# Kernel optimization log

Measured on AMD Instinct MI355X. Metric: run time of the kernel, lower is better.

The kernel has to match this reference:

```python
import jax, jax.numpy as jnp
import numpy as np

T, B = 384, 128
IN_DIM, HID, OUT_DIM = 512, 1024, 512


def _lstm_step(h, c, x_t, Wx, Wh, b):
    # x_t: [B, D], h/c: [B, H]; gates order: i, f, g, o
    gates = x_t @ Wx + h @ Wh + b  # [B, 4H]
    i, f, g, o = jnp.split(gates, 4, axis=-1)
    c_new = jax.nn.sigmoid(f) * c + jax.nn.sigmoid(i) * jnp.tanh(g)
    h_new = jax.nn.sigmoid(o) * jnp.tanh(c_new)
    return h_new, c_new


def setup_inputs() -> dict:
    key = jax.random.key(0)
    ks = jax.random.split(key, 9)
    s_in = 1.0 / np.sqrt(IN_DIM)
    s_h = 1.0 / np.sqrt(HID)
    s_o = 1.0 / np.sqrt(OUT_DIM)
    return {
        "x": jax.random.normal(ks[0], (T, B, IN_DIM), dtype=jnp.float32),
        "hidden_state": jnp.zeros((1, B, HID), dtype=jnp.float32),
        "cell_state": jnp.zeros((1, B, HID), dtype=jnp.float32),
        "enc_Wx": jax.random.normal(ks[1], (IN_DIM, 4 * HID), dtype=jnp.float32) * s_in,
        "enc_Wh": jax.random.normal(ks[2], (HID, 4 * HID), dtype=jnp.float32) * s_h,
        "enc_b": jnp.zeros((4 * HID,), dtype=jnp.float32),
        "dec_Wx": jax.random.normal(ks[3], (OUT_DIM, 4 * HID), dtype=jnp.float32) * s_o,
        "dec_Wh": jax.random.normal(ks[4], (HID, 4 * HID), dtype=jnp.float32) * s_h,
        "dec_b": jnp.zeros((4 * HID,), dtype=jnp.float32),
        "fc_W": jax.random.normal(ks[5], (HID, OUT_DIM), dtype=jnp.float32) * s_h,
        "fc_b": jnp.zeros((OUT_DIM,), dtype=jnp.float32),
    }


def reference(x, hidden_state, cell_state, enc_Wx, enc_Wh, enc_b,
              dec_Wx, dec_Wh, dec_b, fc_W, fc_b):
    # ---- encoder: run LSTM over T steps, keep only final hidden state ----
    h0, c0 = hidden_state[0], cell_state[0]  # [B, H]

    def enc_step(carry, x_t):
        h, c = carry
        h, c = _lstm_step(h, c, x_t, enc_Wx, enc_Wh, enc_b)
        return (h, c), None

    (h_enc, _), _ = jax.lax.scan(enc_step, (h0, c0), x)

    y0 = jnp.zeros((B, OUT_DIM), dtype=x.dtype)
    c_dec0 = jnp.zeros((B, HID), dtype=x.dtype)

    def dec_step(carry, _):
        y, h, c = carry
        h, c = _lstm_step(h, c, y, dec_Wx, dec_Wh, dec_b)
        y = jax.nn.softmax(h @ fc_W + fc_b, axis=-1)  # softmax over dim=2
        return (y, h, c), y

    _, output = jax.lax.scan(dec_step, (y0, h_enc, c_dec0), None, length=T)
    return output  # [T, B, OUT_DIM]
```

## Files before the change

### kernel.cpp

```cpp
#include <hip/hip_runtime.h>


#define TS 384

typedef __attribute__((ext_vector_type(8))) short bf16x8;
typedef __attribute__((ext_vector_type(4))) float f32x4;

#define WS_XR 4096u
#define XR_SLOT 262144u
#define WS_HP (WS_XR + 4u*XR_SLOT)
#define HP_BUF 524288u
#define WS_FPN (WS_HP + 2u*HP_BUF)
#define WS_TOTAL (WS_FPN + 2097152u)

__device__ __forceinline__ unsigned short bf16r(float v) {
  unsigned u = __float_as_uint(v);
  u += 0x7FFFu + ((u >> 16) & 1u);
  return (unsigned short)(u >> 16);
}
__device__ __forceinline__ float bf2f(unsigned short h) {
  return __uint_as_float(((unsigned)h) << 16);
}
__device__ __forceinline__ void split2(float v, short& hi, short& lo) {
  unsigned short h = bf16r(v);
  float r = v - bf2f(h);
  hi = (short)h; lo = (short)bf16r(r);
}
__device__ __forceinline__ float sigm(float v)  { return 1.0f / (1.0f + __expf(-v)); }
__device__ __forceinline__ float tanhfa(float v){ return 1.0f - 2.0f / (__expf(2.0f*v) + 1.0f); }

__device__ __forceinline__ void st_u64(void* p, unsigned long long v) {
  __hip_atomic_store((unsigned long long*)p, v, __ATOMIC_RELAXED, __HIP_MEMORY_SCOPE_AGENT);
}
__device__ __forceinline__ void st_f32(float* p, float v) {
  __hip_atomic_store(p, v, __ATOMIC_RELAXED, __HIP_MEMORY_SCOPE_AGENT);
}
__device__ __forceinline__ float ld_f32(const float* p) {
  return __hip_atomic_load(p, __ATOMIC_RELAXED, __HIP_MEMORY_SCOPE_AGENT);
}
union FRAG { unsigned long long q[2]; bf16x8 v; };
__device__ __forceinline__ bf16x8 ld_frag(const short* base) {
  FRAG u;
  u.q[0] = __hip_atomic_load((const unsigned long long*)base, __ATOMIC_RELAXED, __HIP_MEMORY_SCOPE_AGENT);
  u.q[1] = __hip_atomic_load((const unsigned long long*)(base + 4), __ATOMIC_RELAXED, __HIP_MEMORY_SCOPE_AGENT);
  return u.v;
}

__device__ __forceinline__ void setflag(unsigned* flag, unsigned val) {
  asm volatile("s_waitcnt vmcnt(0)" ::: "memory");
  __syncthreads();
  if (threadIdx.x == 0) {
    __hip_atomic_store(flag, val, __ATOMIC_RELAXED, __HIP_MEMORY_SCOPE_AGENT);
    asm volatile("s_waitcnt vmcnt(0)" ::: "memory");
  }
}
__device__ __forceinline__ void waitflags(const unsigned* flags, int nflags,
                                          unsigned target, bool fence, int* sDead) {
  if (threadIdx.x < 64) {
    const int i = threadIdx.x;
    const bool act = (i * 4) < nflags;
    const unsigned long long* q = (const unsigned long long*)(flags + i * 4);
    unsigned spins = 0;
    for (;;) {
      bool ok = true;
      if (act) {
        unsigned long long q0 = __hip_atomic_load(q, __ATOMIC_RELAXED, __HIP_MEMORY_SCOPE_AGENT);
        unsigned long long q1 = __hip_atomic_load(q + 1, __ATOMIC_RELAXED, __HIP_MEMORY_SCOPE_AGENT);
        ok = ((unsigned)q0 >= target) && ((unsigned)(q0 >> 32) >= target)
          && ((unsigned)q1 >= target) && ((unsigned)(q1 >> 32) >= target);
      }
      if (__all(ok)) break;
      __builtin_amdgcn_s_sleep(1);
      if (++spins > (1u << 19)) { if (i == 0) *sDead = 1; break; }
    }
    if (fence) __builtin_amdgcn_fence(__ATOMIC_ACQUIRE, "agent");
  }
  __syncthreads();
}

__device__ void load_gate_weights(const float* __restrict__ Wx, const float* __restrict__ Wh,
                                  int p, short* sBh, short* sBl) {
  for (int idx = threadIdx.x; idx < 24576; idx += 1024) {
    int j = idx & 7, l = (idx >> 3) & 63, kb = idx >> 9;
    int k = kb * 32 + ((l >> 4) << 3) + j;
    int c = l & 15;
    int gcol = (c >> 2) * 1024 + p * 4 + (c & 3);
    float wv = (k < 512) ? Wx[(size_t)k * 4096 + gcol]
                         : Wh[(size_t)(k - 512) * 4096 + gcol];
    short hi, lo; split2(wv, hi, lo);
    sBh[idx] = hi; sBl[idx] = lo;
  }
}
__device__ void load_fc_weights(const float* __restrict__ fcW, int kg, int cg,
                                short* sFh, short* sFl) {
  for (int idx = threadIdx.x; idx < 4096; idx += 1024) {
    int j = idx & 7, l = (idx >> 3) & 63, kb = idx >> 9;
    int unit = kg * 256 + kb * 32 + ((l >> 4) << 3) + j;
    int col = cg * 16 + (l & 15);
    short hi, lo; split2(fcW[(size_t)unit * 512 + col], hi, lo);
    sFh[idx] = hi; sFl[idx] = lo;
  }
}

__device__ __forceinline__ void gg(const short* AHs, const short* ALs,
    const short* BHs, const short* BLs, int mt, int l,
    int kbA0, int kbB0, int nkb, f32x4* acc)
{
  const bf16x8* AH = (const bf16x8*)AHs;
  const bf16x8* AL = (const bf16x8*)ALs;
  const bf16x8* BH = (const bf16x8*)BHs;
  const bf16x8* BL = (const bf16x8*)BLs;
  #pragma unroll 2
  for (int i = 0; i < nkb; i += 2) {
    int ka = kbA0 + i, kb = kbB0 + i;
    bf16x8 ah0 = AH[(ka * 8 + mt) * 64 + l];
    bf16x8 al0 = AL[(ka * 8 + mt) * 64 + l];
    bf16x8 bh0 = BH[kb * 64 + l];
    bf16x8 bl0 = BL[kb * 64 + l];
    bf16x8 ah1 = AH[((ka + 1) * 8 + mt) * 64 + l];
    bf16x8 al1 = AL[((ka + 1) * 8 + mt) * 64 + l];
    bf16x8 bh1 = BH[(kb + 1) * 64 + l];
    bf16x8 bl1 = BL[(kb + 1) * 64 + l];
    acc[0] = __builtin_amdgcn_mfma_f32_16x16x32_bf16(ah0, bh0, acc[0], 0, 0, 0);
    acc[1] = __builtin_amdgcn_mfma_f32_16x16x32_bf16(ah0, bl0, acc[1], 0, 0, 0);
    acc[2] = __builtin_amdgcn_mfma_f32_16x16x32_bf16(al0, bh0, acc[2], 0, 0, 0);
    acc[3] = __builtin_amdgcn_mfma_f32_16x16x32_bf16(ah1, bh1, acc[3], 0, 0, 0);
    acc[4] = __builtin_amdgcn_mfma_f32_16x16x32_bf16(ah1, bl1, acc[4], 0, 0, 0);
    acc[5] = __builtin_amdgcn_mfma_f32_16x16x32_bf16(al1, bh1, acc[5], 0, 0, 0);
  }
}
__device__ __forceinline__ void gg_finish(f32x4* acc, int kh, int mt, int l,
                                          float* LDSgate) {
  f32x4 s = (acc[0] + acc[3]) + ((acc[1] + acc[4]) + (acc[2] + acc[5]));
  const int col = l & 15, r0 = mt * 16 + ((l >> 4) << 2);
  float* plane = LDSgate + kh * 2176;
  #pragma unroll
  for (int j = 0; j < 4; ++j) plane[(r0 + j) * 17 + col] = s[j];
}

__device__ __forceinline__ void conv_x(const float* __restrict__ xsrc,
                                       short* dstH, short* dstL, int p, int t) {
  if (t < 32) {
    int g = p * 32 + t;
    int l = g & 63, mt = (g >> 6) & 7, kb = g >> 9;
    int row = mt * 16 + (l & 15), k = kb * 32 + ((l >> 4) << 3);
    const float* xs = xsrc + (size_t)row * 512 + k;
    unsigned long long h64[2] = {0, 0}, l64[2] = {0, 0};
    #pragma unroll
    for (int j = 0; j < 8; ++j) {
      short hi, lo; split2(xs[j], hi, lo);
      h64[j >> 2] |= (unsigned long long)(unsigned short)hi << ((j & 3) * 16);
      l64[j >> 2] |= (unsigned long long)(unsigned short)lo << ((j & 3) * 16);
    }
    int off = g * 8;
    st_u64(dstH + off, h64[0]); st_u64(dstH + off + 4, h64[1]);
    st_u64(dstL + off, l64[0]); st_u64(dstL + off + 4, l64[1]);
  }
}

__global__ void __launch_bounds__(1024, 1)
lstm6(const float* __restrict__ x, const float* __restrict__ h0p,
      const float* __restrict__ c0p, const float* __restrict__ eWx,
      const float* __restrict__ eWh, const float* __restrict__ eb,
      const float* __restrict__ dWx, const float* __restrict__ dWh,
      const float* __restrict__ db, const float* __restrict__ fcW,
      const float* __restrict__ fcb, float* __restrict__ out,
      char* __restrict__ ws)
{
  __shared__ __align__(16) short sBh[24576], sBl[24576];
  __shared__ __align__(16) short sFh[4096], sFl[4096];
  __shared__ float LDSgate[2 * 2176];
  __shared__ unsigned hsplit[512];
  __shared__ float ybuf[512];
  __shared__ float red[16];
  __shared__ int sDead;

  const int p = blockIdx.x, t = threadIdx.x;
  const int w = t >> 6, l = t & 63;
  const int mt = w & 7, kh = w >> 3;
  if (t == 0) sDead = 0;

  unsigned* hflag = (unsigned*)ws;
  unsigned* yflag = (unsigned*)(ws + 1024);
  unsigned* fflag = (unsigned*)(ws + 2048);

  short* xrH[4]; short* xrL[4];
  #pragma unroll
  for (int s4 = 0; s4 < 4; ++s4) {
    xrH[s4] = (short*)(ws + WS_XR + s4 * XR_SLOT);
    xrL[s4] = (short*)(ws + WS_XR + s4 * XR_SLOT + 131072u);
  }
  short* hpH[2]; short* hpL[2];
  #pragma unroll
  for (int b2 = 0; b2 < 2; ++b2) {
    hpH[b2] = (short*)(ws + WS_HP + b2 * HP_BUF);
    hpL[b2] = (short*)(ws + WS_HP + b2 * HP_BUF + 262144u);
  }
  float* fp = (float*)(ws + WS_FPN);

  const int row_pw = t & 127, u_pw = (t >> 7) & 3;

  load_gate_weights(eWx, eWh, p, sBh, sBl);
  conv_x(x, xrH[0], xrL[0], p, t);
  conv_x(x + 65536, xrH[1], xrL[1], p, t);
  if (t < 64) {
    int hg = p * 64 + t;
    int ll = hg & 63, mtt = (hg >> 6) & 7, hk = hg >> 9;
    int row = mtt * 16 + (ll & 15), k = hk * 32 + ((ll >> 4) << 3);
    const float* hs = h0p + (size_t)row * 1024 + k;
    unsigned long long h64[2] = {0, 0}, l64[2] = {0, 0};
    #pragma unroll
    for (int j = 0; j < 8; ++j) {
      short hi, lo; split2(hs[j], hi, lo);
      h64[j >> 2] |= (unsigned long long)(unsigned short)hi << ((j & 3) * 16);
      l64[j >> 2] |= (unsigned long long)(unsigned short)lo << ((j & 3) * 16);
    }
    int off = hg * 8;
    st_u64(hpH[0] + off, h64[0]); st_u64(hpH[0] + off + 4, h64[1]);
    st_u64(hpL[0] + off, l64[0]); st_u64(hpL[0] + off + 4, l64[1]);
  }
  float creg = 0.f, bq0 = 0.f, bq1 = 0.f, bq2 = 0.f, bq3 = 0.f;
  if (t < 512) {
    creg = c0p[(size_t)row_pw * 1024 + p * 4 + u_pw];
    bq0 = eb[0 * 1024 + p * 4 + u_pw];
    bq1 = eb[1 * 1024 + p * 4 + u_pw];
    bq2 = eb[2 * 1024 + p * 4 + u_pw];
    bq3 = eb[3 * 1024 + p * 4 + u_pw];
  }
  setflag(&hflag[p], 1u);
  waitflags(hflag, 256, 1u, true, &sDead);
  if (sDead) return;

  for (int st = 0; st < TS; ++st) {
    int rb = st & 1, wb = rb ^ 1, xs = st & 3;
    f32x4 z = {0.f, 0.f, 0.f, 0.f};
    f32x4 acc[6] = {z, z, z, z, z, z};
    gg(xrH[xs], xrL[xs], sBh, sBl, mt, l, kh * 8, kh * 8, 8, acc);
    waitflags(hflag, 256, (unsigned)(st + 1), true, &sDead);
    if (sDead) return;
    gg(hpH[rb], hpL[rb], sBh, sBl, mt, l, kh * 16, 16 + kh * 16, 16, acc);
    gg_finish(acc, kh, mt, l, LDSgate);
    __syncthreads();
    if (t < 512) {
      float g0 = LDSgate[row_pw * 17 + 0  + u_pw] + LDSgate[2176 + row_pw * 17 + 0  + u_pw] + bq0;
      float g1 = LDSgate[row_pw * 17 + 4  + u_pw] + LDSgate[2176 + row_pw * 17 + 4  + u_pw] + bq1;
      float g2 = LDSgate[row_pw * 17 + 8  + u_pw] + LDSgate[2176 + row_pw * 17 + 8  + u_pw] + bq2;
      float g3 = LDSgate[row_pw * 17 + 12 + u_pw] + LDSgate[2176 + row_pw * 17 + 12 + u_pw] + bq3;
      creg = sigm(g1) * creg + sigm(g0) * tanhfa(g2);
      float h = sigm(g3) * tanhfa(creg);
      short hi, lo; split2(h, hi, lo);
      hsplit[u_pw * 128 + row_pw] = ((unsigned)(unsigned short)hi << 16) | (unsigned short)lo;
    }
    if (st + 2 < TS)
      conv_x(x + (size_t)(st + 2) * 65536, xrH[(st + 2) & 3], xrL[(st + 2) & 3], p, t);
    __syncthreads();
    if (t < 128) {
      int r = t;
      unsigned w0 = hsplit[r], w1 = hsplit[128 + r], w2 = hsplit[256 + r], w3 = hsplit[384 + r];
      unsigned long long hi64 = (unsigned long long)(w0 >> 16)
        | ((unsigned long long)(w1 >> 16) << 16)
        | ((unsigned long long)(w2 >> 16) << 32)
        | ((unsigned long long)(w3 >> 16) << 48);
      unsigned long long lo64 = (unsigned long long)(w0 & 0xFFFFu)
        | ((unsigned long long)(w1 & 0xFFFFu) << 16)
        | ((unsigned long long)(w2 & 0xFFFFu) << 32)
        | ((unsigned long long)(w3 & 0xFFFFu) << 48);
      int hk = p >> 3, mtt = r >> 4;
      int lane_ = (((p >> 1) & 3) << 4) | (r & 15);
      int off = ((hk * 8 + mtt) * 64 + lane_) * 8 + (p & 1) * 4;
      st_u64(hpH[wb] + off, hi64);
      st_u64(hpL[wb] + off, lo64);
    }
    setflag(&hflag[p], (unsigned)(st + 2));
  }

  load_gate_weights(dWx, dWh, p, sBh, sBl);
  if (p >= 128) load_fc_weights(fcW, (p - 128) >> 5, (p - 128) & 31, sFh, sFl);
  if (t < 32) {
    int off = (p * 32 + t) * 8;
    st_u64(xrH[0] + off, 0ull); st_u64(xrH[0] + off + 4, 0ull);
    st_u64(xrL[0] + off, 0ull); st_u64(xrL[0] + off + 4, 0ull);
  }
  creg = 0.0f;
  if (t < 512) {
    bq0 = db[0 * 1024 + p * 4 + u_pw];
    bq1 = db[1 * 1024 + p * 4 + u_pw];
    bq2 = db[2 * 1024 + p * 4 + u_pw];
    bq3 = db[3 * 1024 + p * 4 + u_pw];
  }
  float fcb_r = (t < 512) ? fcb[t] : 0.f;
  setflag(&hflag[p], (unsigned)(TS + 2));

  const unsigned DB = (unsigned)(TS + 2);
  for (int st = 0; st < TS; ++st) {
    int rb = st & 1, wb = rb ^ 1;
    int ys = st & 1, yw = ys ^ 1;
    f32x4 z = {0.f, 0.f, 0.f, 0.f};
    f32x4 acc[6] = {z, z, z, z, z, z};
    waitflags(hflag, 256, DB + (unsigned)st, true, &sDead);
    if (sDead) return;
    gg(hpH[rb], hpL[rb], sBh, sBl, mt, l, kh * 16, 16 + kh * 16, 16, acc);
    waitflags(yflag, 128, (unsigned)st, false, &sDead);
    if (sDead) return;
    gg(xrH[ys], xrL[ys], sBh, sBl, mt, l, kh * 8, kh * 8, 8, acc);
    gg_finish(acc, kh, mt, l, LDSgate);
    __syncthreads();
    if (t < 512) {
      float g0 = LDSgate[row_pw * 17 + 0  + u_pw] + LDSgate[2176 + row_pw * 17 + 0  + u_pw] + bq0;
      float g1 = LDSgate[row_pw * 17 + 4  + u_pw] + LDSgate[2176 + row_pw * 17 + 4  + u_pw] + bq1;
      float g2 = LDSgate[row_pw * 17 + 8  + u_pw] + LDSgate[2176 + row_pw * 17 + 8  + u_pw] + bq2;
      float g3 = LDSgate[row_pw * 17 + 12 + u_pw] + LDSgate[2176 + row_pw * 17 + 12 + u_pw] + bq3;
      creg = sigm(g1) * creg + sigm(g0) * tanhfa(g2);
      float h = sigm(g3) * tanhfa(creg);
      short hi, lo; split2(h, hi, lo);
      hsplit[u_pw * 128 + row_pw] = ((unsigned)(unsigned short)hi << 16) | (unsigned short)lo;
    }
    __syncthreads();
    if (t < 128) {
      int r = t;
      unsigned w0 = hsplit[r], w1 = hsplit[128 + r], w2 = hsplit[256 + r], w3 = hsplit[384 + r];
      unsigned long long hi64 = (unsigned long long)(w0 >> 16)
        | ((unsigned long long)(w1 >> 16) << 16)
        | ((unsigned long long)(w2 >> 16) << 32)
        | ((unsigned long long)(w3 >> 16) << 48);
      unsigned long long lo64 = (unsigned long long)(w0 & 0xFFFFu)
        | ((unsigned long long)(w1 & 0xFFFFu) << 16)
        | ((unsigned long long)(w2 & 0xFFFFu) << 32)
        | ((unsigned long long)(w3 & 0xFFFFu) << 48);
      int hk = p >> 3, mtt = r >> 4;
      int lane_ = (((p >> 1) & 3) << 4) | (r & 15);
      int off = ((hk * 8 + mtt) * 64 + lane_) * 8 + (p & 1) * 4;
      st_u64(hpH[wb] + off, hi64);
      st_u64(hpL[wb] + off, lo64);
    }
    setflag(&hflag[p], DB + (unsigned)(st + 1));

    if (p >= 128) {
      const int f = p - 128, kg = f >> 5, cg = f & 31;
      waitflags(hflag + kg * 64, 64, DB + (unsigned)(st + 1), false, &sDead);
      if (sDead) return;
      {
        const bf16x8* FB = (const bf16x8*)sFh;
        const bf16x8* FL = (const bf16x8*)sFl;
        f32x4 a0 = z, a1 = z, a2 = z;
        #pragma unroll
        for (int kb = 0; kb < 4; ++kb) {
          int gkb = kg * 8 + kh * 4 + kb;
          bf16x8 ah = ld_frag(hpH[wb] + ((gkb * 8 + mt) * 64 + l) * 8);
          bf16x8 al = ld_frag(hpL[wb] + ((gkb * 8 + mt) * 64 + l) * 8);
          bf16x8 bh = FB[(kh * 4 + kb) * 64 + l];
          bf16x8 bl = FL[(kh * 4 + kb) * 64 + l];
          a0 = __builtin_amdgcn_mfma_f32_16x16x32_bf16(ah, bh, a0, 0, 0, 0);
          a1 = __builtin_amdgcn_mfma_f32_16x16x32_bf16(ah, bl, a1, 0, 0, 0);
          a2 = __builtin_amdgcn_mfma_f32_16x16x32_bf16(al, bh, a2, 0, 0, 0);
        }
        f32x4 s = a0 + (a1 + a2);
        int slice = kg * 2 + kh;
        int col = cg * 16 + (l & 15), r0 = mt * 16 + ((l >> 4) << 2);
        #pragma unroll
        for (int j = 0; j < 4; ++j)
          st_f32(&fp[(size_t)(slice * 128 + r0 + j) * 512 + col], s[j]);
      }
      setflag(&fflag[f], (unsigned)(st + 1));
    } else {
      waitflags(fflag, 128, (unsigned)(st + 1), false, &sDead);
      if (sDead) return;
      float v = 0.f, e = 0.f, mx;
      if (t < 512) {
        v = fcb_r;
        #pragma unroll
        for (int s8 = 0; s8 < 8; ++s8)
          v += ld_f32(&fp[(size_t)(s8 * 128 + p) * 512 + t]);
        mx = v;
        #pragma unroll
        for (int o = 32; o > 0; o >>= 1) mx = fmaxf(mx, __shfl_xor(mx, o));
        if (l == 0) red[w] = mx;
      }
      __syncthreads();
      if (t < 512) {
        mx = red[0];
        #pragma unroll
        for (int i = 1; i < 8; ++i) mx = fmaxf(mx, red[i]);
        e = __expf(v - mx);
        float ss = e;
        #pragma unroll
        for (int o = 32; o > 0; o >>= 1) ss += __shfl_xor(ss, o);
        if (l == 0) red[8 + w] = ss;
      }
      __syncthreads();
      if (t < 512) {
        float ss = (red[8] + red[9]) + (red[10] + red[11])
                 + (red[12] + red[13]) + (red[14] + red[15]);
        float y = e / ss;
        out[((size_t)st * 128 + p) * 512 + t] = y;
        ybuf[t] = y;
      }
      __syncthreads();
      if (t < 64) {
        int kb = t >> 2, seg = t & 3;
        int k = kb * 32 + seg * 8;
        int lane_ = (seg << 4) | (p & 15), mtt = p >> 4;
        int off = ((kb * 8 + mtt) * 64 + lane_) * 8;
        unsigned long long h64[2] = {0, 0}, l64[2] = {0, 0};
        #pragma unroll
        for (int j = 0; j < 8; ++j) {
          short hi, lo; split2(ybuf[k + j], hi, lo);
          h64[j >> 2] |= (unsigned long long)(unsigned short)hi << ((j & 3) * 16);
          l64[j >> 2] |= (unsigned long long)(unsigned short)lo << ((j & 3) * 16);
        }
        st_u64(xrH[yw] + off, h64[0]); st_u64(xrH[yw] + off + 4, h64[1]);
        st_u64(xrL[yw] + off, l64[0]); st_u64(xrL[yw] + off + 4, l64[1]);
      }
      setflag(&yflag[p], (unsigned)(st + 1));
    }
  }
}

extern "C" void kernel_launch(void* const* d_in, const int* in_sizes, int n_in,
                              void* d_out, int out_size, void* d_ws, size_t ws_size,
                              hipStream_t stream) {
  const float* x   = (const float*)d_in[0];
  const float* h0  = (const float*)d_in[1];
  const float* c0  = (const float*)d_in[2];
  const float* eWx = (const float*)d_in[3];
  const float* eWh = (const float*)d_in[4];
  const float* eb  = (const float*)d_in[5];
  const float* dWx = (const float*)d_in[6];
  const float* dWh = (const float*)d_in[7];
  const float* db  = (const float*)d_in[8];
  const float* fcW = (const float*)d_in[9];
  const float* fcb = (const float*)d_in[10];
  float* out = (float*)d_out;

  if (ws_size < (size_t)WS_TOTAL) {
    hipMemsetAsync(d_out, 0xFF, (size_t)out_size * sizeof(float), stream);
    return;
  }
  hipMemsetAsync(d_ws, 0, 4096, stream);
  hipLaunchKernelGGL(lstm6, dim3(256), dim3(1024), 0, stream,
                     x, h0, c0, eWx, eWh, eb, dWx, dWh, db, fcW, fcb, out,
                     (char*)d_ws);
}
```

Before: 15.77 ms.

## Split gate GEMM across 4-block groups by K and batch, reducing partials via global memory

Each block now owns 16 hidden units for all four gates and a quarter of the K dimension, instead of 4 units over the full K. Four blocks form a group, write partial gate sums to a global workspace, and synchronize through new per-block flags before each block applies the nonlinearity to its 32 batch rows. As a result each block waits only on the h flags of one K-slice rather than all 256 blocks, and the x conversion is moved onto otherwise idle threads. The trade-off is extra global traffic for partial sums plus an additional intra-group flag handshake on every step.

```diff
diff --git a/kernel.cpp b/kernel.cpp
--- a/kernel.cpp
+++ b/kernel.cpp
@@ -10,8 +10,11 @@
 #define XR_SLOT 262144u
 #define WS_HP (WS_XR + 4u*XR_SLOT)
 #define HP_BUF 524288u
-#define WS_FPN (WS_HP + 2u*HP_BUF)
+#define WS_C  (WS_HP + 2u*HP_BUF)
+#define WS_FPN (WS_C + 16777216u)
 #define WS_TOTAL (WS_FPN + 2097152u)
+
+#define MFMA __builtin_amdgcn_mfma_f32_16x16x32_bf16
 
 __device__ __forceinline__ unsigned short bf16r(float v) {
   unsigned u = __float_as_uint(v);
@@ -54,8 +57,17 @@
     asm volatile("s_waitcnt vmcnt(0)" ::: "memory");
   }
 }
+__device__ __forceinline__ void release_set(unsigned* flag, unsigned val) {
+  asm volatile("s_waitcnt vmcnt(0)" ::: "memory");
+  __syncthreads();
+  if (threadIdx.x == 0) {
+    __builtin_amdgcn_fence(__ATOMIC_RELEASE, "agent");
+    __hip_atomic_store(flag, val, __ATOMIC_RELAXED, __HIP_MEMORY_SCOPE_AGENT);
+    asm volatile("s_waitcnt vmcnt(0)" ::: "memory");
+  }
+}
 __device__ __forceinline__ void waitflags(const unsigned* flags, int nflags,
-                                          unsigned target, bool fence, int* sDead) {
+                                          unsigned target, int* sDead) {
   if (threadIdx.x < 64) {
     const int i = threadIdx.x;
     const bool act = (i * 4) < nflags;
@@ -73,26 +85,44 @@
       __builtin_amdgcn_s_sleep(1);
       if (++spins > (1u << 19)) { if (i == 0) *sDead = 1; break; }
     }
+  }
+  __syncthreads();
+}
+__device__ __forceinline__ void wait4(const unsigned* f4, unsigned target,
+                                      bool fence, int* sDead) {
+  if (threadIdx.x == 0) {
+    unsigned spins = 0;
+    for (;;) {
+      unsigned long long q0 = __hip_atomic_load((const unsigned long long*)f4,
+                                 __ATOMIC_RELAXED, __HIP_MEMORY_SCOPE_AGENT);
+      unsigned long long q1 = __hip_atomic_load((const unsigned long long*)(f4 + 2),
+                                 __ATOMIC_RELAXED, __HIP_MEMORY_SCOPE_AGENT);
+      if ((unsigned)q0 >= target && (unsigned)(q0 >> 32) >= target &&
+          (unsigned)q1 >= target && (unsigned)(q1 >> 32) >= target) break;
+      __builtin_amdgcn_s_sleep(1);
+      if (++spins > (1u << 19)) { *sDead = 1; break; }
+    }
     if (fence) __builtin_amdgcn_fence(__ATOMIC_ACQUIRE, "agent");
   }
   __syncthreads();
 }
 
-__device__ void load_gate_weights(const float* __restrict__ Wx, const float* __restrict__ Wh,
-                                  int p, short* sBh, short* sBl) {
+__device__ void load_gw(const float* __restrict__ Wx, const float* __restrict__ Wh,
+                        int g, int s, short* sBh, short* sBl) {
   for (int idx = threadIdx.x; idx < 24576; idx += 1024) {
-    int j = idx & 7, l = (idx >> 3) & 63, kb = idx >> 9;
-    int k = kb * 32 + ((l >> 4) << 3) + j;
-    int c = l & 15;
-    int gcol = (c >> 2) * 1024 + p * 4 + (c & 3);
-    float wv = (k < 512) ? Wx[(size_t)k * 4096 + gcol]
-                         : Wh[(size_t)(k - 512) * 4096 + gcol];
+    int j = idx & 7, l = (idx >> 3) & 63, chunk = idx >> 9;
+    int nt = chunk / 12, kbl = chunk % 12;
+    int gcol = nt * 1024 + g * 16 + (l & 15);
+    int kin = ((l >> 4) << 3) + j;
+    float wv;
+    if (kbl < 4) wv = Wx[(size_t)(s * 128 + kbl * 32 + kin) * 4096 + gcol];
+    else         wv = Wh[(size_t)(s * 256 + (kbl - 4) * 32 + kin) * 4096 + gcol];
     short hi, lo; split2(wv, hi, lo);
     sBh[idx] = hi; sBl[idx] = lo;
   }
 }
-__device__ void load_fc_weights(const float* __restrict__ fcW, int kg, int cg,
-                                short* sFh, short* sFl) {
+__device__ void load_fcw(const float* __restrict__ fcW, int kg, int cg,
+                         short* sFh, short* sFl) {
   for (int idx = threadIdx.x; idx < 4096; idx += 1024) {
     int j = idx & 7, l = (idx >> 3) & 63, kb = idx >> 9;
     int unit = kg * 256 + kb * 32 + ((l >> 4) << 3) + j;
@@ -102,46 +132,41 @@
   }
 }
 
-__device__ __forceinline__ void gg(const short* AHs, const short* ALs,
-    const short* BHs, const short* BLs, int mt, int l,
-    int kbA0, int kbB0, int nkb, f32x4* acc)
+template<int NKB>
+__device__ __forceinline__ void gg_part(const short* AH_, const short* AL_,
+    const short* sBh, const short* sBl, int mt, int l,
+    int kbgA0, int kblB0, f32x4* acc)
 {
-  const bf16x8* AH = (const bf16x8*)AHs;
-  const bf16x8* AL = (const bf16x8*)ALs;
-  const bf16x8* BH = (const bf16x8*)BHs;
-  const bf16x8* BL = (const bf16x8*)BLs;
-  #pragma unroll 2
-  for (int i = 0; i < nkb; i += 2) {
-    int ka = kbA0 + i, kb = kbB0 + i;
-    bf16x8 ah0 = AH[(ka * 8 + mt) * 64 + l];
-    bf16x8 al0 = AL[(ka * 8 + mt) * 64 + l];
-    bf16x8 bh0 = BH[kb * 64 + l];
-    bf16x8 bl0 = BL[kb * 64 + l];
-    bf16x8 ah1 = AH[((ka + 1) * 8 + mt) * 64 + l];
-    bf16x8 al1 = AL[((ka + 1) * 8 + mt) * 64 + l];
-    bf16x8 bh1 = BH[(kb + 1) * 64 + l];
-    bf16x8 bl1 = BL[(kb + 1) * 64 + l];
-    acc[0] = __builtin_amdgcn_mfma_f32_16x16x32_bf16(ah0, bh0, acc[0], 0, 0, 0);
-    acc[1] = __builtin_amdgcn_mfma_f32_16x16x32_bf16(ah0, bl0, acc[1], 0, 0, 0);
-    acc[2] = __builtin_amdgcn_mfma_f32_16x16x32_bf16(al0, bh0, acc[2], 0, 0, 0);
-    acc[3] = __builtin_amdgcn_mfma_f32_16x16x32_bf16(ah1, bh1, acc[3], 0, 0, 0);
-    acc[4] = __builtin_amdgcn_mfma_f32_16x16x32_bf16(ah1, bl1, acc[4], 0, 0, 0);
-    acc[5] = __builtin_amdgcn_mfma_f32_16x16x32_bf16(al1, bh1, acc[5], 0, 0, 0);
-  }
-}
-__device__ __forceinline__ void gg_finish(f32x4* acc, int kh, int mt, int l,
-                                          float* LDSgate) {
-  f32x4 s = (acc[0] + acc[3]) + ((acc[1] + acc[4]) + (acc[2] + acc[5]));
-  const int col = l & 15, r0 = mt * 16 + ((l >> 4) << 2);
-  float* plane = LDSgate + kh * 2176;
+  const bf16x8* AH = (const bf16x8*)AH_;
+  const bf16x8* AL = (const bf16x8*)AL_;
+  const bf16x8* BH = (const bf16x8*)sBh;
+  const bf16x8* BL = (const bf16x8*)sBl;
+  bf16x8 ah = AH[(kbgA0 * 8 + mt) * 64 + l];
+  bf16x8 al = AL[(kbgA0 * 8 + mt) * 64 + l];
   #pragma unroll
-  for (int j = 0; j < 4; ++j) plane[(r0 + j) * 17 + col] = s[j];
+  for (int i = 0; i < NKB; ++i) {
+    bf16x8 ahn = ah, aln = al;
+    if (i + 1 < NKB) {
+      ahn = AH[((kbgA0 + i + 1) * 8 + mt) * 64 + l];
+      aln = AL[((kbgA0 + i + 1) * 8 + mt) * 64 + l];
+    }
+    const int kbl = kblB0 + i;
+    #pragma unroll
+    for (int nt = 0; nt < 4; ++nt) {
+      bf16x8 bh = BH[(nt * 12 + kbl) * 64 + l];
+      bf16x8 bl = BL[(nt * 12 + kbl) * 64 + l];
+      acc[nt * 3 + 0] = MFMA(ah, bh, acc[nt * 3 + 0], 0, 0, 0);
+      acc[nt * 3 + 1] = MFMA(ah, bl, acc[nt * 3 + 1], 0, 0, 0);
+      acc[nt * 3 + 2] = MFMA(al, bh, acc[nt * 3 + 2], 0, 0, 0);
+    }
+    ah = ahn; al = aln;
+  }
 }
 
 __device__ __forceinline__ void conv_x(const float* __restrict__ xsrc,
-                                       short* dstH, short* dstL, int p, int t) {
-  if (t < 32) {
-    int g = p * 32 + t;
+                                       short* dstH, short* dstL, int b, int tl) {
+  if (tl < 32) {
+    int g = b * 32 + tl;
     int l = g & 63, mt = (g >> 6) & 7, kb = g >> 9;
     int row = mt * 16 + (l & 15), k = kb * 32 + ((l >> 4) << 3);
     const float* xs = xsrc + (size_t)row * 512 + k;
@@ -159,7 +184,7 @@
 }
 
 __global__ void __launch_bounds__(1024, 1)
-lstm6(const float* __restrict__ x, const float* __restrict__ h0p,
+lstm7(const float* __restrict__ x, const float* __restrict__ h0p,
       const float* __restrict__ c0p, const float* __restrict__ eWx,
       const float* __restrict__ eWh, const float* __restrict__ eb,
       const float* __restrict__ dWx, const float* __restrict__ dWh,
@@ -169,20 +194,21 @@
 {
   __shared__ __align__(16) short sBh[24576], sBl[24576];
   __shared__ __align__(16) short sFh[4096], sFl[4096];
-  __shared__ float LDSgate[2 * 2176];
   __shared__ unsigned hsplit[512];
   __shared__ float ybuf[512];
   __shared__ float red[16];
   __shared__ int sDead;
 
-  const int p = blockIdx.x, t = threadIdx.x;
+  const int b = blockIdx.x, t = threadIdx.x;
   const int w = t >> 6, l = t & 63;
   const int mt = w & 7, kh = w >> 3;
+  const int g = b >> 2, s = b & 3;
   if (t == 0) sDead = 0;
 
   unsigned* hflag = (unsigned*)ws;
   unsigned* yflag = (unsigned*)(ws + 1024);
   unsigned* fflag = (unsigned*)(ws + 2048);
+  unsigned* pflag = (unsigned*)(ws + 3072);
 
   short* xrH[4]; short* xrL[4];
   #pragma unroll
@@ -196,15 +222,18 @@
     hpH[b2] = (short*)(ws + WS_HP + b2 * HP_BUF);
     hpL[b2] = (short*)(ws + WS_HP + b2 * HP_BUF + 262144u);
   }
+  float* Call = (float*)(ws + WS_C);
+  float* Cb   = Call + (size_t)b * 16384 + kh * 8192;
+  const float* Cg = Call + (size_t)(g * 4) * 16384;
   float* fp = (float*)(ws + WS_FPN);
 
-  const int row_pw = t & 127, u_pw = (t >> 7) & 3;
-
-  load_gate_weights(eWx, eWh, p, sBh, sBl);
-  conv_x(x, xrH[0], xrL[0], p, t);
-  conv_x(x + 65536, xrH[1], xrL[1], p, t);
+  const int u_pw = t >> 5, rl_pw = t & 31;
+
+  load_gw(eWx, eWh, g, s, sBh, sBl);
+  conv_x(x, xrH[0], xrL[0], b, t);
+  conv_x(x + 65536, xrH[1], xrL[1], b, t);
   if (t < 64) {
-    int hg = p * 64 + t;
+    int hg = b * 64 + t;
     int ll = hg & 63, mtt = (hg >> 6) & 7, hk = hg >> 9;
     int row = mtt * 16 + (ll & 15), k = hk * 32 + ((ll >> 4) << 3);
     const float* hs = h0p + (size_t)row * 1024 + k;
@@ -221,123 +250,158 @@
   }
   float creg = 0.f, bq0 = 0.f, bq1 = 0.f, bq2 = 0.f, bq3 = 0.f;
   if (t < 512) {
-    creg = c0p[(size_t)row_pw * 1024 + p * 4 + u_pw];
-    bq0 = eb[0 * 1024 + p * 4 + u_pw];
-    bq1 = eb[1 * 1024 + p * 4 + u_pw];
-    bq2 = eb[2 * 1024 + p * 4 + u_pw];
-    bq3 = eb[3 * 1024 + p * 4 + u_pw];
-  }
-  setflag(&hflag[p], 1u);
-  waitflags(hflag, 256, 1u, true, &sDead);
+    int row = s * 32 + rl_pw, ug = g * 16 + u_pw;
+    creg = c0p[(size_t)row * 1024 + ug];
+    bq0 = eb[0 * 1024 + ug]; bq1 = eb[1 * 1024 + ug];
+    bq2 = eb[2 * 1024 + ug]; bq3 = eb[3 * 1024 + ug];
+  }
+  setflag(&hflag[b], 1u);
+  waitflags(hflag, 256, 1u, &sDead);
+  if (t == 0) __builtin_amdgcn_fence(__ATOMIC_ACQUIRE, "agent");
+  __syncthreads();
   if (sDead) return;
 
   for (int st = 0; st < TS; ++st) {
-    int rb = st & 1, wb = rb ^ 1, xs = st & 3;
+    const int rb = st & 1, wb = rb ^ 1;
     f32x4 z = {0.f, 0.f, 0.f, 0.f};
-    f32x4 acc[6] = {z, z, z, z, z, z};
-    gg(xrH[xs], xrL[xs], sBh, sBl, mt, l, kh * 8, kh * 8, 8, acc);
-    waitflags(hflag, 256, (unsigned)(st + 1), true, &sDead);
+    f32x4 acc[12] = {z, z, z, z, z, z, z, z, z, z, z, z};
+    gg_part<2>(xrH[st & 3], xrL[st & 3], sBh, sBl, mt, l, s * 4 + kh * 2, kh * 2, acc);
+    waitflags(hflag + s * 64, 64, (unsigned)(st + 1), &sDead);
     if (sDead) return;
-    gg(hpH[rb], hpL[rb], sBh, sBl, mt, l, kh * 16, 16 + kh * 16, 16, acc);
-    gg_finish(acc, kh, mt, l, LDSgate);
-    __syncthreads();
+    gg_part<4>(hpH[rb], hpL[rb], sBh, sBl, mt, l, s * 8 + kh * 4, 4 + kh * 4, acc);
+    if ((g >> 4) != s) {
+      wait4(hflag + g * 4, (unsigned)(st + 1), false, &sDead);
+      if (sDead) return;
+    }
+    #pragma unroll
+    for (int nt = 0; nt < 4; ++nt) {
+      f32x4 sv = acc[nt * 3] + (acc[nt * 3 + 1] + acc[nt * 3 + 2]);
+      *(f32x4*)&Cb[(nt * 16 + (l & 15)) * 128 + mt * 16 + ((l >> 4) << 2)] = sv;
+    }
+    release_set(&pflag[b], (unsigned)(st + 1));
+    wait4(pflag + g * 4, (unsigned)(st + 1), true, &sDead);
+    if (sDead) return;
     if (t < 512) {
-      float g0 = LDSgate[row_pw * 17 + 0  + u_pw] + LDSgate[2176 + row_pw * 17 + 0  + u_pw] + bq0;
-      float g1 = LDSgate[row_pw * 17 + 4  + u_pw] + LDSgate[2176 + row_pw * 17 + 4  + u_pw] + bq1;
-      float g2 = LDSgate[row_pw * 17 + 8  + u_pw] + LDSgate[2176 + row_pw * 17 + 8  + u_pw] + bq2;
-      float g3 = LDSgate[row_pw * 17 + 12 + u_pw] + LDSgate[2176 + row_pw * 17 + 12 + u_pw] + bq3;
+      int row = s * 32 + rl_pw;
+      float g0 = bq0, g1 = bq1, g2 = bq2, g3 = bq3;
+      #pragma unroll
+      for (int sl = 0; sl < 4; ++sl)
+        #pragma unroll
+        for (int kp = 0; kp < 2; ++kp) {
+          const float* Cp = Cg + sl * 16384 + kp * 8192 + row;
+          g0 += Cp[(0 * 16 + u_pw) * 128];
+          g1 += Cp[(1 * 16 + u_pw) * 128];
+          g2 += Cp[(2 * 16 + u_pw) * 128];
+          g3 += Cp[(3 * 16 + u_pw) * 128];
+        }
       creg = sigm(g1) * creg + sigm(g0) * tanhfa(g2);
       float h = sigm(g3) * tanhfa(creg);
       short hi, lo; split2(h, hi, lo);
-      hsplit[u_pw * 128 + row_pw] = ((unsigned)(unsigned short)hi << 16) | (unsigned short)lo;
-    }
-    if (st + 2 < TS)
-      conv_x(x + (size_t)(st + 2) * 65536, xrH[(st + 2) & 3], xrL[(st + 2) & 3], p, t);
+      hsplit[u_pw * 32 + rl_pw] = ((unsigned)(unsigned short)hi << 16) | (unsigned short)lo;
+    } else if (st + 2 < TS) {
+      conv_x(x + (size_t)(st + 2) * 65536, xrH[(st + 2) & 3], xrL[(st + 2) & 3], b, t - 512);
+    }
     __syncthreads();
-    if (t < 128) {
-      int r = t;
-      unsigned w0 = hsplit[r], w1 = hsplit[128 + r], w2 = hsplit[256 + r], w3 = hsplit[384 + r];
-      unsigned long long hi64 = (unsigned long long)(w0 >> 16)
-        | ((unsigned long long)(w1 >> 16) << 16)
-        | ((unsigned long long)(w2 >> 16) << 32)
-        | ((unsigned long long)(w3 >> 16) << 48);
-      unsigned long long lo64 = (unsigned long long)(w0 & 0xFFFFu)
-        | ((unsigned long long)(w1 & 0xFFFFu) << 16)
-        | ((unsigned long long)(w2 & 0xFFFFu) << 32)
-        | ((unsigned long long)(w3 & 0xFFFFu) << 48);
-      int hk = p >> 3, mtt = r >> 4;
-      int lane_ = (((p >> 1) & 3) << 4) | (r & 15);
-      int off = ((hk * 8 + mtt) * 64 + lane_) * 8 + (p & 1) * 4;
-      st_u64(hpH[wb] + off, hi64);
-      st_u64(hpL[wb] + off, lo64);
-    }
-    setflag(&hflag[p], (unsigned)(st + 2));
-  }
-
-  load_gate_weights(dWx, dWh, p, sBh, sBl);
-  if (p >= 128) load_fc_weights(fcW, (p - 128) >> 5, (p - 128) & 31, sFh, sFl);
+    if (t < 64) {
+      int rl = t >> 1, seg = t & 1;
+      int row = s * 32 + rl;
+      int k0 = g * 16 + seg * 8;
+      int kbg = k0 >> 5, kseg = (k0 >> 3) & 3;
+      int lane_ = (kseg << 4) | (row & 15);
+      int off = ((kbg * 8 + (row >> 4)) * 64 + lane_) * 8;
+      unsigned long long h64[2] = {0, 0}, l64[2] = {0, 0};
+      #pragma unroll
+      for (int j = 0; j < 8; ++j) {
+        unsigned v = hsplit[(seg * 8 + j) * 32 + rl];
+        h64[j >> 2] |= (unsigned long long)(v >> 16) << ((j & 3) * 16);
+        l64[j >> 2] |= (unsigned long long)(v & 0xFFFFu) << ((j & 3) * 16);
+      }
+      st_u64(hpH[wb] + off, h64[0]); st_u64(hpH[wb] + off + 4, h64[1]);
+      st_u64(hpL[wb] + off, l64[0]); st_u64(hpL[wb] + off + 4, l64[1]);
+    }
+    setflag(&hflag[b], (unsigned)(st + 2));
+  }
+
+  load_gw(dWx, dWh, g, s, sBh, sBl);
+  if (b >= 128) load_fcw(fcW, (b - 128) >> 5, (b - 128) & 31, sFh, sFl);
   if (t < 32) {
-    int off = (p * 32 + t) * 8;
+    int off = (b * 32 + t) * 8;
     st_u64(xrH[0] + off, 0ull); st_u64(xrH[0] + off + 4, 0ull);
     st_u64(xrL[0] + off, 0ull); st_u64(xrL[0] + off + 4, 0ull);
   }
   creg = 0.0f;
   if (t < 512) {
-    bq0 = db[0 * 1024 + p * 4 + u_pw];
-    bq1 = db[1 * 1024 + p * 4 + u_pw];
-    bq2 = db[2 * 1024 + p * 4 + u_pw];
-    bq3 = db[3 * 1024 + p * 4 + u_pw];
+    int ug = g * 16 + u_pw;
+    bq0 = db[0 * 1024 + ug]; bq1 = db[1 * 1024 + ug];
+    bq2 = db[2 * 1024 + ug]; bq3 = db[3 * 1024 + ug];
   }
   float fcb_r = (t < 512) ? fcb[t] : 0.f;
-  setflag(&hflag[p], (unsigned)(TS + 2));
+  setflag(&hflag[b], (unsigned)(TS + 2));
 
   const unsigned DB = (unsigned)(TS + 2);
   for (int st = 0; st < TS; ++st) {
-    int rb = st & 1, wb = rb ^ 1;
-    int ys = st & 1, yw = ys ^ 1;
+    const int rb = st & 1, wb = rb ^ 1;
     f32x4 z = {0.f, 0.f, 0.f, 0.f};
-    f32x4 acc[6] = {z, z, z, z, z, z};
-    waitflags(hflag, 256, DB + (unsigned)st, true, &sDead);
+    f32x4 acc[12] = {z, z, z, z, z, z, z, z, z, z, z, z};
+    waitflags(hflag + s * 64, 64, DB + (unsigned)st, &sDead);
     if (sDead) return;
-    gg(hpH[rb], hpL[rb], sBh, sBl, mt, l, kh * 16, 16 + kh * 16, 16, acc);
-    waitflags(yflag, 128, (unsigned)st, false, &sDead);
+    gg_part<4>(hpH[rb], hpL[rb], sBh, sBl, mt, l, s * 8 + kh * 4, 4 + kh * 4, acc);
+    waitflags(yflag, 128, (unsigned)st, &sDead);
     if (sDead) return;
-    gg(xrH[ys], xrL[ys], sBh, sBl, mt, l, kh * 8, kh * 8, 8, acc);
-    gg_finish(acc, kh, mt, l, LDSgate);
-    __syncthreads();
+    gg_part<2>(xrH[st & 1], xrL[st & 1], sBh, sBl, mt, l, s * 4 + kh * 2, kh * 2, acc);
+    if ((g >> 4) != s) {
+      wait4(hflag + g * 4, DB + (unsigned)st, false, &sDead);
+      if (sDead) return;
+    }
+    #pragma unroll
+    for (int nt = 0; nt < 4; ++nt) {
+      f32x4 sv = acc[nt * 3] + (acc[nt * 3 + 1] + acc[nt * 3 + 2]);
+      *(f32x4*)&Cb[(nt * 16 + (l & 15)) * 128 + mt * 16 + ((l >> 4) << 2)] = sv;
+    }
+    release_set(&pflag[b], (unsigned)(TS + st + 1));
+    wait4(pflag + g * 4, (unsigned)(TS + st + 1), true, &sDead);
+    if (sDead) return;
     if (t < 512) {
-      float g0 = LDSgate[row_pw * 17 + 0  + u_pw] + LDSgate[2176 + row_pw * 17 + 0  + u_pw] + bq0;
-      float g1 = LDSgate[row_pw * 17 + 4  + u_pw] + LDSgate[2176 + row_pw * 17 + 4  + u_pw] + bq1;
-      float g2 = LDSgate[row_pw * 17 + 8  + u_pw] + LDSgate[2176 + row_pw * 17 + 8  + u_pw] + bq2;
-      float g3 = LDSgate[row_pw * 17 + 12 + u_pw] + LDSgate[2176 + row_pw * 17 + 12 + u_pw] + bq3;
+      int row = s * 32 + rl_pw;
+      float g0 = bq0, g1 = bq1, g2 = bq2, g3 = bq3;
+      #pragma unroll
+      for (int sl = 0; sl < 4; ++sl)
+        #pragma unroll
+        for (int kp = 0; kp < 2; ++kp) {
+          const float* Cp = Cg + sl * 16384 + kp * 8192 + row;
+          g0 += Cp[(0 * 16 + u_pw) * 128];
+          g1 += Cp[(1 * 16 + u_pw) * 128];
+          g2 += Cp[(2 * 16 + u_pw) * 128];
+          g3 += Cp[(3 * 16 + u_pw) * 128];
+        }
       creg = sigm(g1) * creg + sigm(g0) * tanhfa(g2);
       float h = sigm(g3) * tanhfa(creg);
       short hi, lo; split2(h, hi, lo);
-      hsplit[u_pw * 128 + row_pw] = ((unsigned)(unsigned short)hi << 16) | (unsigned short)lo;
+      hsplit[u_pw * 32 + rl_pw] = ((unsigned)(unsigned short)hi << 16) | (unsigned short)lo;
     }
     __syncthreads();
-    if (t < 128) {
-      int r = t;
-      unsigned w0 = hsplit[r], w1 = hsplit[128 + r], w2 = hsplit[256 + r], w3 = hsplit[384 + r];
-      unsigned long long hi64 = (unsigned long long)(w0 >> 16)
-        | ((unsigned long long)(w1 >> 16) << 16)
-        | ((unsigned long long)(w2 >> 16) << 32)
-        | ((unsigned long long)(w3 >> 16) << 48);
-      unsigned long long lo64 = (unsigned long long)(w0 & 0xFFFFu)
-        | ((unsigned long long)(w1 & 0xFFFFu) << 16)
-        | ((unsigned long long)(w2 & 0xFFFFu) << 32)
-        | ((unsigned long long)(w3 & 0xFFFFu) << 48);
-      int hk = p >> 3, mtt = r >> 4;
-      int lane_ = (((p >> 1) & 3) << 4) | (r & 15);
-      int off = ((hk * 8 + mtt) * 64 + lane_) * 8 + (p & 1) * 4;
-      st_u64(hpH[wb] + off, hi64);
-      st_u64(hpL[wb] + off, lo64);
-    }
-    setflag(&hflag[p], DB + (unsigned)(st + 1));
-
-    if (p >= 128) {
-      const int f = p - 128, kg = f >> 5, cg = f & 31;
-      waitflags(hflag + kg * 64, 64, DB + (unsigned)(st + 1), false, &sDead);
+    if (t < 64) {
+      int rl = t >> 1, seg = t & 1;
+      int row = s * 32 + rl;
+      int k0 = g * 16 + seg * 8;
+      int kbg = k0 >> 5, kseg = (k0 >> 3) & 3;
+      int lane_ = (kseg << 4) | (row & 15);
+      int off = ((kbg * 8 + (row >> 4)) * 64 + lane_) * 8;
+      unsigned long long h64[2] = {0, 0}, l64[2] = {0, 0};
+      #pragma unroll
+      for (int j = 0; j < 8; ++j) {
+        unsigned v = hsplit[(seg * 8 + j) * 32 + rl];
+        h64[j >> 2] |= (unsigned long long)(v >> 16) << ((j & 3) * 16);
+        l64[j >> 2] |= (unsigned long long)(v & 0xFFFFu) << ((j & 3) * 16);
+      }
+      st_u64(hpH[wb] + off, h64[0]); st_u64(hpH[wb] + off + 4, h64[1]);
+      st_u64(hpL[wb] + off, l64[0]); st_u64(hpL[wb] + off + 4, l64[1]);
+    }
+    setflag(&hflag[b], DB + (unsigned)(st + 1));
+
+    if (b >= 128) {
+      const int f = b - 128, kg = f >> 5, cg = f & 31;
+      waitflags(hflag + kg * 64, 64, DB + (unsigned)(st + 1), &sDead);
       if (sDead) return;
       {
         const bf16x8* FB = (const bf16x8*)sFh;
@@ -350,27 +414,27 @@
           bf16x8 al = ld_frag(hpL[wb] + ((gkb * 8 + mt) * 64 + l) * 8);
           bf16x8 bh = FB[(kh * 4 + kb) * 64 + l];
           bf16x8 bl = FL[(kh * 4 + kb) * 64 + l];
-          a0 = __builtin_amdgcn_mfma_f32_16x16x32_bf16(ah, bh, a0, 0, 0, 0);
-          a1 = __builtin_amdgcn_mfma_f32_16x16x32_bf16(ah, bl, a1, 0, 0, 0);
-          a2 = __builtin_amdgcn_mfma_f32_16x16x32_bf16(al, bh, a2, 0, 0, 0);
+          a0 = MFMA(ah, bh, a0, 0, 0, 0);
+          a1 = MFMA(ah, bl, a1, 0, 0, 0);
+          a2 = MFMA(al, bh, a2, 0, 0, 0);
         }
-        f32x4 s = a0 + (a1 + a2);
+        f32x4 sv = a0 + (a1 + a2);
         int slice = kg * 2 + kh;
         int col = cg * 16 + (l & 15), r0 = mt * 16 + ((l >> 4) << 2);
         #pragma unroll
         for (int j = 0; j < 4; ++j)
-          st_f32(&fp[(size_t)(slice * 128 + r0 + j) * 512 + col], s[j]);
+          st_f32(&fp[(size_t)(slice * 128 + r0 + j) * 512 + col], sv[j]);
       }
       setflag(&fflag[f], (unsigned)(st + 1));
     } else {
-      waitflags(fflag, 128, (unsigned)(st + 1), false, &sDead);
+      waitflags(fflag, 128, (unsigned)(st + 1), &sDead);
       if (sDead) return;
       float v = 0.f, e = 0.f, mx;
       if (t < 512) {
         v = fcb_r;
         #pragma unroll
         for (int s8 = 0; s8 < 8; ++s8)
-          v += ld_f32(&fp[(size_t)(s8 * 128 + p) * 512 + t]);
+          v += ld_f32(&fp[(size_t)(s8 * 128 + b) * 512 + t]);
         mx = v;
         #pragma unroll
         for (int o = 32; o > 0; o >>= 1) mx = fmaxf(mx, __shfl_xor(mx, o));
@@ -392,15 +456,16 @@
         float ss = (red[8] + red[9]) + (red[10] + red[11])
                  + (red[12] + red[13]) + (red[14] + red[15]);
         float y = e / ss;
-        out[((size_t)st * 128 + p) * 512 + t] = y;
+        out[((size_t)st * 128 + b) * 512 + t] = y;
         ybuf[t] = y;
       }
       __syncthreads();
       if (t < 64) {
         int kb = t >> 2, seg = t & 3;
         int k = kb * 32 + seg * 8;
-        int lane_ = (seg << 4) | (p & 15), mtt = p >> 4;
+        int lane_ = (seg << 4) | (b & 15), mtt = b >> 4;
         int off = ((kb * 8 + mtt) * 64 + lane_) * 8;
+        int yw = (st & 1) ^ 1;
         unsigned long long h64[2] = {0, 0}, l64[2] = {0, 0};
         #pragma unroll
         for (int j = 0; j < 8; ++j) {
@@ -411,7 +476,7 @@
         st_u64(xrH[yw] + off, h64[0]); st_u64(xrH[yw] + off + 4, h64[1]);
         st_u64(xrL[yw] + off, l64[0]); st_u64(xrL[yw] + off + 4, l64[1]);
       }
-      setflag(&yflag[p], (unsigned)(st + 1));
+      setflag(&yflag[b], (unsigned)(st + 1));
     }
   }
 }
@@ -437,7 +502,7 @@
     return;
   }
   hipMemsetAsync(d_ws, 0, 4096, stream);
-  hipLaunchKernelGGL(lstm6, dim3(256), dim3(1024), 0, stream,
+  hipLaunchKernelGGL(lstm7, dim3(256), dim3(1024), 0, stream,
                      x, h0, c0, eWx, eWh, eb, dWx, dWh, db, fcW, fcb, out,
                      (char*)d_ws);
 }
```

Measured after the change: 35.51 ms. 2.25x slower.
